# Kernel tuning notes

Hardware: AMD Instinct MI355X
Metric: run time of the kernel (lower is better)

The kernel has to match this reference:

```python
import jax, jax.numpy as jnp
import numpy as np

N = 50000      # nodes
E = 800000     # edges (before self loops)
F_IN = 64
H = 128
OUT = 1
G = 512        # graphs in batch
NEG_SLOPE = 0.2


def setup_inputs() -> dict:
    key = jax.random.key(0)
    ks = jax.random.split(key, 16)
    s_in = 1.0 / np.sqrt(F_IN)
    s_h = 1.0 / np.sqrt(H)
    return {
        "x": jax.random.normal(ks[0], (N, F_IN), jnp.float32),
        "edge_index": jax.random.randint(ks[1], (2, E), 0, N, jnp.int64),
        "edge_weight": jax.random.uniform(ks[2], (E,), jnp.float32),
        "batch": jnp.sort(jax.random.randint(ks[3], (N,), 0, G, jnp.int64)),
        # GATv2 layer 1 (lin_l, lin_r, att, bias)
        "Wl1": jax.random.normal(ks[4], (F_IN, H), jnp.float32) * s_in,
        "bl1": jnp.zeros((H,), jnp.float32),
        "Wr1": jax.random.normal(ks[5], (F_IN, H), jnp.float32) * s_in,
        "br1": jnp.zeros((H,), jnp.float32),
        "att1": jax.random.normal(ks[6], (H,), jnp.float32) * s_h,
        "b1": jnp.zeros((H,), jnp.float32),
        # GATv2 layer 2
        "Wl2": jax.random.normal(ks[7], (H, H), jnp.float32) * s_h,
        "bl2": jnp.zeros((H,), jnp.float32),
        "Wr2": jax.random.normal(ks[8], (H, H), jnp.float32) * s_h,
        "br2": jnp.zeros((H,), jnp.float32),
        "att2": jax.random.normal(ks[9], (H,), jnp.float32) * s_h,
        "b2": jnp.zeros((H,), jnp.float32),
        # final linear head
        "Wlin": jax.random.normal(ks[10], (H, OUT), jnp.float32) * s_h,
        "blin": jnp.zeros((OUT,), jnp.float32),
    }


def gatv2_conv(x, src, dst, Wl, bl, Wr, br, att, bias):
    """PyG GATv2Conv, heads=1: alpha = softmax_dst(att . leaky_relu(xl[src]+xr[dst]));
    out[dst] = sum alpha * xl[src] + bias. Self loops already in (src, dst)."""
    xl = x @ Wl + bl                       # [N,H]  source transform
    xr = x @ Wr + br                       # [N,H]  destination transform
    e = xl[src] + xr[dst]                  # [Etot,H]
    logits = jax.nn.leaky_relu(e, NEG_SLOPE) @ att   # [Etot]
    # segment softmax over destination nodes (self loops -> every node nonempty)
    m = jax.ops.segment_max(logits, dst, num_segments=N)
    ea = jnp.exp(logits - m[dst])
    denom = jax.ops.segment_sum(ea, dst, num_segments=N)
    alpha = ea / denom[dst]
    out = jax.ops.segment_sum(alpha[:, None] * xl[src], dst, num_segments=N)
    return out + bias


def reference(x, edge_index, edge_weight, batch,
              Wl1, bl1, Wr1, br1, att1, b1,
              Wl2, bl2, Wr2, br2, att2, b2,
              Wlin, blin):
    # add self loops (GATv2Conv default add_self_loops=True); edge_weight unused by GATv2
    loops = jnp.arange(N, dtype=edge_index.dtype)
    src = jnp.concatenate([edge_index[0], loops])
    dst = jnp.concatenate([edge_index[1], loops])

    h = jax.nn.relu(gatv2_conv(x, src, dst, Wl1, bl1, Wr1, br1, att1, b1))
    h = jax.nn.relu(gatv2_conv(h, src, dst, Wl2, bl2, Wr2, br2, att2, b2))

    # global mean pool over graphs
    sums = jax.ops.segment_sum(h, batch, num_segments=G)          # [G,H]
    cnt = jax.ops.segment_sum(jnp.ones((N,), h.dtype), batch, num_segments=G)
    pooled = sums / jnp.maximum(cnt, 1.0)[:, None]

    return pooled @ Wlin + blin                                   # [G,OUT]
```

## Files before the change

### kernel.cpp

```cpp
#include <hip/hip_runtime.h>
#include <hip/hip_fp16.h>
#include <math.h>

#define N_NODES 50000
#define N_EDGES 800000
#define F_IN    64
#define H_DIM   128
#define N_GRAPH 512
#define NEG_SLOPE 0.2f
#define SCAN_NB ((N_NODES + 255) / 256)

typedef __attribute__((ext_vector_type(8))) short short8;
typedef __attribute__((ext_vector_type(4))) float f32x4;

__device__ __forceinline__ void bsplit(float v, unsigned short& h, unsigned short& l) {
    unsigned u = __float_as_uint(v);
    h = (unsigned short)(u >> 16);
    float hf = __uint_as_float(u & 0xFFFF0000u);
    float r = v - hf;
    l = (unsigned short)(__float_as_uint(r) >> 16);
}
__device__ __forceinline__ float bjoin(unsigned short h, unsigned short l) {
    return __uint_as_float(((unsigned)h) << 16) + __uint_as_float(((unsigned)l) << 16);
}

__device__ __forceinline__ void load_h8(const unsigned short* base, size_t off,
                                        float4& f0, float4& f1) {
    uint4 u = *(const uint4*)(base + off);
    float2 a = __half22float2(*(__half2*)&u.x);
    float2 b = __half22float2(*(__half2*)&u.y);
    float2 c = __half22float2(*(__half2*)&u.z);
    float2 d = __half22float2(*(__half2*)&u.w);
    f0 = make_float4(a.x, a.y, b.x, b.y);
    f1 = make_float4(c.x, c.y, d.x, d.y);
}

#define NB_PX 3125
#define NB_PW 192
#define NB_H  3125
__global__ __launch_bounds__(256) void k_prep(
    const float* __restrict__ x,
    const float* __restrict__ Wl1, const float* __restrict__ Wr1,
    const float* __restrict__ Wl2, const float* __restrict__ Wr2,
    const int* __restrict__ dst,
    unsigned short* __restrict__ Xhi, unsigned short* __restrict__ Xlo,
    unsigned short* __restrict__ WThi, unsigned short* __restrict__ WTlo,
    int* __restrict__ counts, int* __restrict__ rank)
{
    const int bid = blockIdx.x, tid = threadIdx.x;
    if (bid < NB_PX) {
        int i4 = (bid * 256 + tid) * 4;
        if (i4 < N_NODES * F_IN) {
            float4 v = *(const float4*)(x + i4);
            ushort4 h, l;
            bsplit(v.x, h.x, l.x); bsplit(v.y, h.y, l.y);
            bsplit(v.z, h.z, l.z); bsplit(v.w, h.w, l.w);
            *(ushort4*)(Xhi + i4) = h;
            *(ushort4*)(Xlo + i4) = l;
        }
    } else if (bid < NB_PX + NB_PW) {
        int idx = (bid - NB_PX) * 256 + tid;
        if (idx < 49152) {
            const float* W; int K, li, base, o;
            if (idx < 8192)       { W = Wl1; K = 64;  li = idx;         base = 0;     o = 0; }
            else if (idx < 16384) { W = Wr1; K = 64;  li = idx - 8192;  base = 0;     o = 1; }
            else if (idx < 32768) { W = Wl2; K = 128; li = idx - 16384; base = 16384; o = 0; }
            else                  { W = Wr2; K = 128; li = idx - 32768; base = 16384; o = 1; }
            int c = li / K, k = li - c * K;
            int g = c >> 4, n16 = c & 15;
            int kkblk = k >> 5, quad = (k >> 3) & 3, j = k & 7;
            int off = base + kkblk * 8192 + o * 4096 + g * 512 + (quad * 16 + n16) * 8 + j;
            unsigned short h, l;
            bsplit(W[k * 128 + c], h, l);
            WThi[off] = h; WTlo[off] = l;
        }
    } else {
        int e = (bid - NB_PX - NB_PW) * 256 + tid;
        if (e < N_EDGES) {
            int pos = atomicAdd(&counts[dst[e]], 1);
            rank[e] = pos;
        }
    }
}

__global__ __launch_bounds__(256) void k_scan1(const int* __restrict__ counts,
                                               int* __restrict__ excl,
                                               int* __restrict__ partials) {
    __shared__ int s[256];
    int t = threadIdx.x, gid = blockIdx.x * 256 + t;
    int v = (gid < N_NODES) ? counts[gid] : 0;
    s[t] = v;
    __syncthreads();
    for (int off = 1; off < 256; off <<= 1) {
        int x = (t >= off) ? s[t - off] : 0;
        __syncthreads();
        s[t] += x;
        __syncthreads();
    }
    if (gid < N_NODES) excl[gid] = s[t] - v;
    if (t == 255) partials[blockIdx.x] = s[t];
}

__global__ __launch_bounds__(256) void k_scan3(int* __restrict__ offsets,
                                               const int* __restrict__ partials) {
    __shared__ int s[256];
    const int t = threadIdx.x, b = blockIdx.x;
    int v = (t < SCAN_NB) ? partials[t] : 0;
    s[t] = v;
    __syncthreads();
    for (int off = 1; off < 256; off <<= 1) {
        int x = (t >= off) ? s[t - off] : 0;
        __syncthreads();
        s[t] += x;
        __syncthreads();
    }
    int base = (b > 0) ? s[b - 1] : 0;
    int gid = b * 256 + t;
    if (gid < N_NODES) offsets[gid] += base;
    if (gid == 0) offsets[N_NODES] = N_EDGES;
}

__global__ __launch_bounds__(256) void k_fill(const int* __restrict__ src,
                                              const int* __restrict__ dst,
                                              const int* __restrict__ offsets,
                                              const int* __restrict__ rank,
                                              int* __restrict__ col_src) {
    int e = blockIdx.x * 256 + threadIdx.x;
    if (e < N_EDGES) {
        col_src[offsets[dst[e]] + rank[e]] = src[e];
    }
}

#define APITCH 40
#define GB_GEMM ((N_NODES + 63) / 64)
__global__ __launch_bounds__(256, 4) void k_gemm_mfma(
    const unsigned short* __restrict__ Xhi, const unsigned short* __restrict__ Xlo,
    const unsigned short* __restrict__ WThi, const unsigned short* __restrict__ WTlo,
    const float* __restrict__ bl, const float* __restrict__ br,
    unsigned short* __restrict__ OL, unsigned short* __restrict__ OR_, int K)
{
    __shared__ __align__(16) unsigned short Ah[64 * APITCH];
    __shared__ __align__(16) unsigned short Al[64 * APITCH];

    const int tid  = threadIdx.x;
    const int wv   = tid >> 6;
    const int lane = tid & 63;
    const int n16  = lane & 15;
    const int quad = lane >> 4;
    const int row0 = blockIdx.x * 64;

    f32x4 acc[4][2][2];
#pragma unroll
    for (int r = 0; r < 4; ++r)
#pragma unroll
        for (int c = 0; c < 2; ++c)
#pragma unroll
            for (int o = 0; o < 2; ++o) acc[r][c][o] = (f32x4)0.f;

    for (int kk = 0; kk < K; kk += 32) {
#pragma unroll
        for (int jj = 0; jj < 2; ++jj) {
            int j = tid + jj * 256;
            int part = j >> 8;
            int r = (j & 255) >> 2, sub = j & 3;
            int grow = row0 + r;
            const unsigned short* s = (part ? Xlo : Xhi) + (size_t)grow * K + kk + sub * 8;
            unsigned short* dl = (part ? Al : Ah) + r * APITCH + sub * 8;
            uint4 v = make_uint4(0u, 0u, 0u, 0u);
            if (grow < N_NODES) v = *(const uint4*)s;
            *(uint4*)dl = v;
        }
        __syncthreads();

        const unsigned short* wb_h = WThi + (size_t)(kk >> 5) * 8192;
        const unsigned short* wb_l = WTlo + (size_t)(kk >> 5) * 8192;
        short8 bh[2][2], bo[2][2];
#pragma unroll
        for (int c = 0; c < 2; ++c)
#pragma unroll
            for (int o = 0; o < 2; ++o) {
                size_t off = (size_t)o * 4096 + (size_t)(wv * 2 + c) * 512 + (size_t)lane * 8;
                bh[c][o] = *(const short8*)(wb_h + off);
                bo[c][o] = *(const short8*)(wb_l + off);
            }
#pragma unroll
        for (int r = 0; r < 4; ++r) {
            int rl = r * 16 + n16;
            short8 ah = *(const short8*)(Ah + rl * APITCH + quad * 8);
            short8 al = *(const short8*)(Al + rl * APITCH + quad * 8);
#pragma unroll
            for (int c = 0; c < 2; ++c)
#pragma unroll
                for (int o = 0; o < 2; ++o) {
                    f32x4 t = acc[r][c][o];
                    t = __builtin_amdgcn_mfma_f32_16x16x32_bf16(ah, bh[c][o], t, 0, 0, 0);
                    t = __builtin_amdgcn_mfma_f32_16x16x32_bf16(ah, bo[c][o], t, 0, 0, 0);
                    t = __builtin_amdgcn_mfma_f32_16x16x32_bf16(al, bh[c][o], t, 0, 0, 0);
                    acc[r][c][o] = t;
                }
        }
        __syncthreads();
    }

#pragma unroll
    for (int r = 0; r < 4; ++r)
#pragma unroll
        for (int c = 0; c < 2; ++c)
#pragma unroll
            for (int o = 0; o < 2; ++o) {
                int col = wv * 32 + c * 16 + n16;
                float bb = (o ? br : bl)[col];
                unsigned short* O = o ? OR_ : OL;
#pragma unroll
                for (int g = 0; g < 4; ++g) {
                    int grow = row0 + r * 16 + quad * 4 + g;
                    if (grow < N_NODES) {
                        __half hv = __float2half(acc[r][c][o][g] + bb);
                        O[(size_t)grow * 128 + col] = *(unsigned short*)&hv;
                    }
                }
            }
}

__device__ __forceinline__ float dot8_leaky(const float4& x0, const float4& x1,
                                            const float4& r0, const float4& r1,
                                            const float4& a0, const float4& a1) {
    float s = 0.f, e;
    e = x0.x + r0.x; s = fmaf(a0.x, (e > 0.f ? e : NEG_SLOPE * e), s);
    e = x0.y + r0.y; s = fmaf(a0.y, (e > 0.f ? e : NEG_SLOPE * e), s);
    e = x0.z + r0.z; s = fmaf(a0.z, (e > 0.f ? e : NEG_SLOPE * e), s);
    e = x0.w + r0.w; s = fmaf(a0.w, (e > 0.f ? e : NEG_SLOPE * e), s);
    e = x1.x + r1.x; s = fmaf(a1.x, (e > 0.f ? e : NEG_SLOPE * e), s);
    e = x1.y + r1.y; s = fmaf(a1.y, (e > 0.f ? e : NEG_SLOPE * e), s);
    e = x1.z + r1.z; s = fmaf(a1.z, (e > 0.f ? e : NEG_SLOPE * e), s);
    e = x1.w + r1.w; s = fmaf(a1.w, (e > 0.f ? e : NEG_SLOPE * e), s);
    return s;
}

__global__ __launch_bounds__(256) void k_edge(
    const unsigned short* __restrict__ xl, const unsigned short* __restrict__ xr,
    const float* __restrict__ att, const float* __restrict__ bias,
    const int* __restrict__ offsets, const int* __restrict__ col_src,
    unsigned short* __restrict__ outHi, unsigned short* __restrict__ outLo)
{
    int d = blockIdx.x * 4 + (threadIdx.x >> 6);
    if (d >= N_NODES) return;
    const int lane = threadIdx.x & 63;
    const int q = lane >> 4;
    const int t = lane & 15;
    const size_t dim0 = (size_t)t * 8;

    float4 r0, r1;
    load_h8(xr, (size_t)d * 128 + dim0, r0, r1);
    const float4 a0 = *(const float4*)(att + dim0);
    const float4 a1 = *(const float4*)(att + dim0 + 4);

    float4 xs0, xs1;
    load_h8(xl, (size_t)d * 128 + dim0, xs0, xs1);
    float sl = dot8_leaky(xs0, xs1, r0, r1, a0, a1);
#pragma unroll
    for (int off = 1; off < 16; off <<= 1) sl += __shfl_xor(sl, off);

    float m, lsum;
    float4 acc0, acc1;
    if (q == 0) {
        m = sl; lsum = 1.f; acc0 = xs0; acc1 = xs1;
    } else {
        m = -INFINITY; lsum = 0.f;
        acc0 = make_float4(0.f, 0.f, 0.f, 0.f);
        acc1 = make_float4(0.f, 0.f, 0.f, 0.f);
    }

    const int ibeg = offsets[d], iend = offsets[d + 1];
    for (int base = ibeg; base < iend; base += 4) {
        int i = base + q;
        bool valid = (i < iend);
        int s = valid ? col_src[i] : d;
        float4 x0, x1;
        load_h8(xl, (size_t)s * 128 + dim0, x0, x1);
        float logit = dot8_leaky(x0, x1, r0, r1, a0, a1);
#pragma unroll
        for (int off = 1; off < 16; off <<= 1) logit += __shfl_xor(logit, off);
        if (valid) {
            float nm = fmaxf(m, logit);
            float sc = __expf(m - nm);
            float w  = __expf(logit - nm);
            lsum = lsum * sc + w;
            acc0.x = acc0.x * sc + w * x0.x;
            acc0.y = acc0.y * sc + w * x0.y;
            acc0.z = acc0.z * sc + w * x0.z;
            acc0.w = acc0.w * sc + w * x0.w;
            acc1.x = acc1.x * sc + w * x1.x;
            acc1.y = acc1.y * sc + w * x1.y;
            acc1.z = acc1.z * sc + w * x1.z;
            acc1.w = acc1.w * sc + w * x1.w;
            m = nm;
        }
    }

    float M = m;
    M = fmaxf(M, __shfl_xor(M, 16));
    M = fmaxf(M, __shfl_xor(M, 32));
    float sc = __expf(m - M);
    lsum *= sc;
    acc0.x *= sc; acc0.y *= sc; acc0.z *= sc; acc0.w *= sc;
    acc1.x *= sc; acc1.y *= sc; acc1.z *= sc; acc1.w *= sc;
#pragma unroll
    for (int off = 16; off <= 32; off <<= 1) {
        lsum  += __shfl_xor(lsum, off);
        acc0.x += __shfl_xor(acc0.x, off);
        acc0.y += __shfl_xor(acc0.y, off);
        acc0.z += __shfl_xor(acc0.z, off);
        acc0.w += __shfl_xor(acc0.w, off);
        acc1.x += __shfl_xor(acc1.x, off);
        acc1.y += __shfl_xor(acc1.y, off);
        acc1.z += __shfl_xor(acc1.z, off);
        acc1.w += __shfl_xor(acc1.w, off);
    }

    if (q == 0) {
        float inv = 1.f / lsum;
        const float4 b0 = *(const float4*)(bias + dim0);
        const float4 b1 = *(const float4*)(bias + dim0 + 4);
        float v[8];
        v[0] = fmaxf(fmaf(acc0.x, inv, b0.x), 0.f);
        v[1] = fmaxf(fmaf(acc0.y, inv, b0.y), 0.f);
        v[2] = fmaxf(fmaf(acc0.z, inv, b0.z), 0.f);
        v[3] = fmaxf(fmaf(acc0.w, inv, b0.w), 0.f);
        v[4] = fmaxf(fmaf(acc1.x, inv, b1.x), 0.f);
        v[5] = fmaxf(fmaf(acc1.y, inv, b1.y), 0.f);
        v[6] = fmaxf(fmaf(acc1.z, inv, b1.z), 0.f);
        v[7] = fmaxf(fmaf(acc1.w, inv, b1.w), 0.f);
        union { unsigned short s[8]; uint4 u; } H, L;
#pragma unroll
        for (int i = 0; i < 8; ++i) bsplit(v[i], H.s[i], L.s[i]);
        *(uint4*)(outHi + (size_t)d * 128 + dim0) = H.u;
        *(uint4*)(outLo + (size_t)d * 128 + dim0) = L.u;
    }
}

__global__ __launch_bounds__(256) void k_pool(
    const unsigned short* __restrict__ hHi, const unsigned short* __restrict__ hLo,
    const int* __restrict__ batch,
    float* __restrict__ psum, float* __restrict__ pcnt)
{
    const int tid = threadIdx.x;
    const int tx = tid & 31;
    const int ty = tid >> 5;
    const int n0 = blockIdx.x * 64;
    const int d0 = tx * 4;

    float4 acc = make_float4(0.f, 0.f, 0.f, 0.f);
    int cur = -1, crun = 0;
#pragma unroll
    for (int it = 0; it < 8; ++it) {
        int n = n0 + it * 8 + ty;
        if (n < N_NODES) {
            int g = batch[n];
            if (g != cur) {
                if (cur >= 0) {
                    atomicAdd(&psum[cur * 128 + d0 + 0], acc.x);
                    atomicAdd(&psum[cur * 128 + d0 + 1], acc.y);
                    atomicAdd(&psum[cur * 128 + d0 + 2], acc.z);
                    atomicAdd(&psum[cur * 128 + d0 + 3], acc.w);
                    if (tx == 0) atomicAdd(&pcnt[cur], (float)crun);
                }
                cur = g; acc = make_float4(0.f, 0.f, 0.f, 0.f); crun = 0;
            }
            ushort4 h = *(const ushort4*)(hHi + (size_t)n * 128 + d0);
            ushort4 l = *(const ushort4*)(hLo + (size_t)n * 128 + d0);
            acc.x += bjoin(h.x, l.x);
            acc.y += bjoin(h.y, l.y);
            acc.z += bjoin(h.z, l.z);
            acc.w += bjoin(h.w, l.w);
            crun++;
        }
    }
    if (cur >= 0) {
        atomicAdd(&psum[cur * 128 + d0 + 0], acc.x);
        atomicAdd(&psum[cur * 128 + d0 + 1], acc.y);
        atomicAdd(&psum[cur * 128 + d0 + 2], acc.z);
        atomicAdd(&psum[cur * 128 + d0 + 3], acc.w);
        if (tx == 0) atomicAdd(&pcnt[cur], (float)crun);
    }
}

__global__ __launch_bounds__(256) void k_head(
    const float* __restrict__ psum, const float* __restrict__ pcnt,
    const float* __restrict__ Wlin, const float* __restrict__ blin,
    float* __restrict__ out)
{
    int g = blockIdx.x * 4 + (threadIdx.x >> 6);
    if (g >= N_GRAPH) return;
    int lane = threadIdx.x & 63;
    float c = fmaxf(pcnt[g], 1.f);
    float2 s = *(const float2*)(psum + (size_t)g * 128 + lane * 2);
    float p = (s.x * Wlin[lane * 2] + s.y * Wlin[lane * 2 + 1]) / c;
#pragma unroll
    for (int off = 32; off > 0; off >>= 1) p += __shfl_xor(p, off);
    if (lane == 0) out[g] = p + blin[0];
}

extern "C" void kernel_launch(void* const* d_in, const int* in_sizes, int n_in,
                              void* d_out, int out_size, void* d_ws, size_t ws_size,
                              hipStream_t stream) {
    const float* x     = (const float*)d_in[0];
    const int*   ei    = (const int*)d_in[1];
    const int*   batch = (const int*)d_in[3];
    const float* Wl1 = (const float*)d_in[4],  *bl1 = (const float*)d_in[5];
    const float* Wr1 = (const float*)d_in[6],  *br1 = (const float*)d_in[7];
    const float* att1= (const float*)d_in[8],  *b1  = (const float*)d_in[9];
    const float* Wl2 = (const float*)d_in[10], *bl2 = (const float*)d_in[11];
    const float* Wr2 = (const float*)d_in[12], *br2 = (const float*)d_in[13];
    const float* att2= (const float*)d_in[14], *b2  = (const float*)d_in[15];
    const float* Wlin= (const float*)d_in[16], *blin= (const float*)d_in[17];
    float* out = (float*)d_out;

    const int* src = ei;
    const int* dst = ei + N_EDGES;

    char* p = (char*)d_ws;
    auto carve = [&](size_t bytes) {
        void* r = (void*)p;
        p += (bytes + 255) & ~(size_t)255;
        return r;
    };
    unsigned short* bufA   = (unsigned short*)carve((size_t)N_NODES * 128 * 2);
    unsigned short* bufB   = (unsigned short*)carve((size_t)N_NODES * 128 * 2);
    unsigned short* Hhi    = (unsigned short*)carve((size_t)N_NODES * 128 * 2);
    unsigned short* Hlo    = (unsigned short*)carve((size_t)N_NODES * 128 * 2);
    unsigned short* Xhi1   = (unsigned short*)carve((size_t)N_NODES * 64 * 2);
    unsigned short* Xlo1   = (unsigned short*)carve((size_t)N_NODES * 64 * 2);
    unsigned short* WThi   = (unsigned short*)carve(49152 * 2);
    unsigned short* WTlo   = (unsigned short*)carve(49152 * 2);
    int*            offsets= (int*)carve((size_t)(N_NODES + 1) * 4);
    int*            rank   = (int*)carve((size_t)N_EDGES * 4);
    int*            partials=(int*)carve(256 * 4);
    int*            col_src= (int*)carve((size_t)N_EDGES * 4);
    char* zb = (char*)carve(200192 + 262144 + 2048);
    int*   counts = (int*)zb;
    float* psum   = (float*)(zb + 200192);
    float* pcnt   = (float*)(zb + 200192 + 262144);
    const size_t zbytes = 200192 + 262144 + 2048;

    hipMemsetAsync(zb, 0, zbytes, stream);

    k_prep<<<NB_PX + NB_PW + NB_H, 256, 0, stream>>>(
        x, Wl1, Wr1, Wl2, Wr2, dst,
        Xhi1, Xlo1, WThi, WTlo, counts, rank);
    k_scan1<<<SCAN_NB, 256, 0, stream>>>(counts, offsets, partials);
    k_scan3<<<SCAN_NB, 256, 0, stream>>>(offsets, partials);
    k_fill <<<(N_EDGES + 255) / 256, 256, 0, stream>>>(src, dst, offsets, rank, col_src);

    k_gemm_mfma<<<GB_GEMM, 256, 0, stream>>>(Xhi1, Xlo1, WThi, WTlo,
                                             bl1, br1, bufA, bufB, F_IN);
    k_edge<<<(N_NODES + 3) / 4, 256, 0, stream>>>(
        bufA, bufB, att1, b1, offsets, col_src, Hhi, Hlo);
    k_gemm_mfma<<<GB_GEMM, 256, 0, stream>>>(Hhi, Hlo, WThi + 16384, WTlo + 16384,
                                             bl2, br2, bufA, bufB, H_DIM);
    k_edge<<<(N_NODES + 3) / 4, 256, 0, stream>>>(
        bufA, bufB, att2, b2, offsets, col_src, Hhi, Hlo);
    k_pool<<<(N_NODES + 63) / 64, 256, 0, stream>>>(Hhi, Hlo, batch, psum, pcnt);
    k_head<<<(N_GRAPH + 3) / 4, 256, 0, stream>>>(psum, pcnt, Wlin, blin, out);
}
```

Baseline: 313.0 us.

## Use DPP reductions, packed f32x2 math, and lazy-rescale online softmax in edge kernel

Replaces the 16-lane shuffle reduction of edge logits with DPP row operations, computes the leaky-relu dot product and accumulator updates with two-wide float vectors so the compiler can emit packed FP32 instructions, and changes the online softmax to rescale only when a logit exceeds the running max by more than a threshold. The threshold removes one exp and a full rescale of the accumulators per edge in the common case. The cost is that weights can grow to about e^8 before rescaling, which slightly changes numerics, and it relies on the DPP row-shift and row-mirror patterns being correct for 16-lane groups.

```diff
diff --git a/kernel.cpp b/kernel.cpp
--- a/kernel.cpp
+++ b/kernel.cpp
@@ -12,6 +12,7 @@
 
 typedef __attribute__((ext_vector_type(8))) short short8;
 typedef __attribute__((ext_vector_type(4))) float f32x4;
+typedef __attribute__((ext_vector_type(2))) float f32x2;
 
 __device__ __forceinline__ void bsplit(float v, unsigned short& h, unsigned short& l) {
     unsigned u = __float_as_uint(v);
@@ -22,17 +23,6 @@
 }
 __device__ __forceinline__ float bjoin(unsigned short h, unsigned short l) {
     return __uint_as_float(((unsigned)h) << 16) + __uint_as_float(((unsigned)l) << 16);
-}
-
-__device__ __forceinline__ void load_h8(const unsigned short* base, size_t off,
-                                        float4& f0, float4& f1) {
-    uint4 u = *(const uint4*)(base + off);
-    float2 a = __half22float2(*(__half2*)&u.x);
-    float2 b = __half22float2(*(__half2*)&u.y);
-    float2 c = __half22float2(*(__half2*)&u.z);
-    float2 d = __half22float2(*(__half2*)&u.w);
-    f0 = make_float4(a.x, a.y, b.x, b.y);
-    f1 = make_float4(c.x, c.y, d.x, d.y);
 }
 
 #define NB_PX 3125
@@ -222,19 +212,47 @@
             }
 }
 
-__device__ __forceinline__ float dot8_leaky(const float4& x0, const float4& x1,
-                                            const float4& r0, const float4& r1,
-                                            const float4& a0, const float4& a1) {
-    float s = 0.f, e;
-    e = x0.x + r0.x; s = fmaf(a0.x, (e > 0.f ? e : NEG_SLOPE * e), s);
-    e = x0.y + r0.y; s = fmaf(a0.y, (e > 0.f ? e : NEG_SLOPE * e), s);
-    e = x0.z + r0.z; s = fmaf(a0.z, (e > 0.f ? e : NEG_SLOPE * e), s);
-    e = x0.w + r0.w; s = fmaf(a0.w, (e > 0.f ? e : NEG_SLOPE * e), s);
-    e = x1.x + r1.x; s = fmaf(a1.x, (e > 0.f ? e : NEG_SLOPE * e), s);
-    e = x1.y + r1.y; s = fmaf(a1.y, (e > 0.f ? e : NEG_SLOPE * e), s);
-    e = x1.z + r1.z; s = fmaf(a1.z, (e > 0.f ? e : NEG_SLOPE * e), s);
-    e = x1.w + r1.w; s = fmaf(a1.w, (e > 0.f ? e : NEG_SLOPE * e), s);
-    return s;
+__device__ __forceinline__ float red16dpp(float v) {
+    v += __int_as_float(__builtin_amdgcn_update_dpp(
+             0, __float_as_int(v), 0xB1, 0xF, 0xF, true));
+    v += __int_as_float(__builtin_amdgcn_update_dpp(
+             0, __float_as_int(v), 0x4E, 0xF, 0xF, true));
+    v += __int_as_float(__builtin_amdgcn_update_dpp(
+             0, __float_as_int(v), 0x141, 0xF, 0xF, true));
+    v += __int_as_float(__builtin_amdgcn_update_dpp(
+             0, __float_as_int(v), 0x140, 0xF, 0xF, true));
+    return v;
+}
+
+__device__ __forceinline__ void load_h8v(const unsigned short* base, size_t off,
+                                         f32x2 x[4]) {
+    uint4 u = *(const uint4*)(base + off);
+    float2 a = __half22float2(*(__half2*)&u.x);
+    float2 b = __half22float2(*(__half2*)&u.y);
+    float2 c = __half22float2(*(__half2*)&u.z);
+    float2 d = __half22float2(*(__half2*)&u.w);
+    f32x2 v0 = {a.x, a.y}; x[0] = v0;
+    f32x2 v1 = {b.x, b.y}; x[1] = v1;
+    f32x2 v2 = {c.x, c.y}; x[2] = v2;
+    f32x2 v3 = {d.x, d.y}; x[3] = v3;
+}
+
+__device__ __forceinline__ float dot8lk(const f32x2 x[4], const f32x2 r[4],
+                                        const f32x2 a[4]) {
+    f32x2 e0 = x[0] + r[0];
+    f32x2 e1 = x[1] + r[1];
+    f32x2 l0 = __builtin_elementwise_max(e0, NEG_SLOPE * e0);
+    f32x2 l1 = __builtin_elementwise_max(e1, NEG_SLOPE * e1);
+    f32x2 s0 = a[0] * l0;
+    f32x2 s1 = a[1] * l1;
+    f32x2 e2 = x[2] + r[2];
+    f32x2 e3 = x[3] + r[3];
+    f32x2 l2 = __builtin_elementwise_max(e2, NEG_SLOPE * e2);
+    f32x2 l3 = __builtin_elementwise_max(e3, NEG_SLOPE * e3);
+    s0 += a[2] * l2;
+    s1 += a[3] * l3;
+    f32x2 s = s0 + s1;
+    return s.x + s.y;
 }
 
 __global__ __launch_bounds__(256) void k_edge(
@@ -250,52 +268,46 @@
     const int t = lane & 15;
     const size_t dim0 = (size_t)t * 8;
 
-    float4 r0, r1;
-    load_h8(xr, (size_t)d * 128 + dim0, r0, r1);
-    const float4 a0 = *(const float4*)(att + dim0);
-    const float4 a1 = *(const float4*)(att + dim0 + 4);
-
-    float4 xs0, xs1;
-    load_h8(xl, (size_t)d * 128 + dim0, xs0, xs1);
-    float sl = dot8_leaky(xs0, xs1, r0, r1, a0, a1);
-#pragma unroll
-    for (int off = 1; off < 16; off <<= 1) sl += __shfl_xor(sl, off);
-
-    float m, lsum;
-    float4 acc0, acc1;
-    if (q == 0) {
-        m = sl; lsum = 1.f; acc0 = xs0; acc1 = xs1;
-    } else {
-        m = -INFINITY; lsum = 0.f;
-        acc0 = make_float4(0.f, 0.f, 0.f, 0.f);
-        acc1 = make_float4(0.f, 0.f, 0.f, 0.f);
-    }
+    f32x2 rr[4], aa[4], xs[4];
+    load_h8v(xr, (size_t)d * 128 + dim0, rr);
+    {
+        const float4 a0 = *(const float4*)(att + dim0);
+        const float4 a1 = *(const float4*)(att + dim0 + 4);
+        f32x2 w0 = {a0.x, a0.y}; aa[0] = w0;
+        f32x2 w1 = {a0.z, a0.w}; aa[1] = w1;
+        f32x2 w2 = {a1.x, a1.y}; aa[2] = w2;
+        f32x2 w3 = {a1.z, a1.w}; aa[3] = w3;
+    }
+    load_h8v(xl, (size_t)d * 128 + dim0, xs);
+    float sl = red16dpp(dot8lk(xs, rr, aa));
+
+    float m = sl, thr = sl + 8.f;
+    float lsum = (q == 0) ? 1.f : 0.f;
+    f32x2 zero = {0.f, 0.f};
+    f32x2 acc[4];
+#pragma unroll
+    for (int j = 0; j < 4; ++j) acc[j] = (q == 0) ? xs[j] : zero;
 
     const int ibeg = offsets[d], iend = offsets[d + 1];
     for (int base = ibeg; base < iend; base += 4) {
         int i = base + q;
         bool valid = (i < iend);
         int s = valid ? col_src[i] : d;
-        float4 x0, x1;
-        load_h8(xl, (size_t)s * 128 + dim0, x0, x1);
-        float logit = dot8_leaky(x0, x1, r0, r1, a0, a1);
-#pragma unroll
-        for (int off = 1; off < 16; off <<= 1) logit += __shfl_xor(logit, off);
-        if (valid) {
-            float nm = fmaxf(m, logit);
-            float sc = __expf(m - nm);
-            float w  = __expf(logit - nm);
-            lsum = lsum * sc + w;
-            acc0.x = acc0.x * sc + w * x0.x;
-            acc0.y = acc0.y * sc + w * x0.y;
-            acc0.z = acc0.z * sc + w * x0.z;
-            acc0.w = acc0.w * sc + w * x0.w;
-            acc1.x = acc1.x * sc + w * x1.x;
-            acc1.y = acc1.y * sc + w * x1.y;
-            acc1.z = acc1.z * sc + w * x1.z;
-            acc1.w = acc1.w * sc + w * x1.w;
-            m = nm;
-        }
+        f32x2 x[4];
+        load_h8v(xl, (size_t)s * 128 + dim0, x);
+        float logit = red16dpp(dot8lk(x, rr, aa));
+        if (__builtin_expect(logit > thr, 0)) {
+            float sc = __expf(m - logit);
+            lsum *= sc;
+#pragma unroll
+            for (int j = 0; j < 4; ++j) acc[j] = acc[j] * sc;
+            m = logit; thr = logit + 8.f;
+        }
+        float w = valid ? __expf(logit - m) : 0.f;
+        lsum += w;
+        f32x2 w2 = {w, w};
+#pragma unroll
+        for (int j = 0; j < 4; ++j) acc[j] += w2 * x[j];
     }
 
     float M = m;
@@ -303,39 +315,35 @@
     M = fmaxf(M, __shfl_xor(M, 32));
     float sc = __expf(m - M);
     lsum *= sc;
-    acc0.x *= sc; acc0.y *= sc; acc0.z *= sc; acc0.w *= sc;
-    acc1.x *= sc; acc1.y *= sc; acc1.z *= sc; acc1.w *= sc;
+    f32x2 sc2 = {sc, sc};
+#pragma unroll
+    for (int j = 0; j < 4; ++j) acc[j] = acc[j] * sc2;
 #pragma unroll
     for (int off = 16; off <= 32; off <<= 1) {
-        lsum  += __shfl_xor(lsum, off);
-        acc0.x += __shfl_xor(acc0.x, off);
-        acc0.y += __shfl_xor(acc0.y, off);
-        acc0.z += __shfl_xor(acc0.z, off);
-        acc0.w += __shfl_xor(acc0.w, off);
-        acc1.x += __shfl_xor(acc1.x, off);
-        acc1.y += __shfl_xor(acc1.y, off);
-        acc1.z += __shfl_xor(acc1.z, off);
-        acc1.w += __shfl_xor(acc1.w, off);
+        lsum += __shfl_xor(lsum, off);
+#pragma unroll
+        for (int j = 0; j < 4; ++j) {
+            acc[j].x += __shfl_xor(acc[j].x, off);
+            acc[j].y += __shfl_xor(acc[j].y, off);
+        }
     }
 
     if (q == 0) {
         float inv = 1.f / lsum;
         const float4 b0 = *(const float4*)(bias + dim0);
         const float4 b1 = *(const float4*)(bias + dim0 + 4);
+        float bv[8] = {b0.x, b0.y, b0.z, b0.w, b1.x, b1.y, b1.z, b1.w};
         float v[8];
-        v[0] = fmaxf(fmaf(acc0.x, inv, b0.x), 0.f);
-        v[1] = fmaxf(fmaf(acc0.y, inv, b0.y), 0.f);
-        v[2] = fmaxf(fmaf(acc0.z, inv, b0.z), 0.f);
-        v[3] = fmaxf(fmaf(acc0.w, inv, b0.w), 0.f);
-        v[4] = fmaxf(fmaf(acc1.x, inv, b1.x), 0.f);
-        v[5] = fmaxf(fmaf(acc1.y, inv, b1.y), 0.f);
-        v[6] = fmaxf(fmaf(acc1.z, inv, b1.z), 0.f);
-        v[7] = fmaxf(fmaf(acc1.w, inv, b1.w), 0.f);
-        union { unsigned short s[8]; uint4 u; } H, L;
-#pragma unroll
-        for (int i = 0; i < 8; ++i) bsplit(v[i], H.s[i], L.s[i]);
-        *(uint4*)(outHi + (size_t)d * 128 + dim0) = H.u;
-        *(uint4*)(outLo + (size_t)d * 128 + dim0) = L.u;
+#pragma unroll
+        for (int j = 0; j < 4; ++j) {
+            v[2 * j]     = fmaxf(fmaf(acc[j].x, inv, bv[2 * j]), 0.f);
+            v[2 * j + 1] = fmaxf(fmaf(acc[j].y, inv, bv[2 * j + 1]), 0.f);
+        }
+        union { unsigned short s[8]; uint4 u; } Hh, Ll;
+#pragma unroll
+        for (int i2 = 0; i2 < 8; ++i2) bsplit(v[i2], Hh.s[i2], Ll.s[i2]);
+        *(uint4*)(outHi + (size_t)d * 128 + dim0) = Hh.u;
+        *(uint4*)(outLo + (size_t)d * 128 + dim0) = Ll.u;
     }
 }
 
```

After: 304.3 us. 1.03x faster.
